# Kernel optimization log

Measured on AMD Instinct MI355X. Metric: run time of the kernel, lower is better.

Reference implementation:

```python
import jax, jax.numpy as jnp
import numpy as np

N = 524288   # frontier nodes processed this step
D = 8        # max_output_degree (padded children per node)
H = 64       # h_size
X = 128      # x_size


def setup_inputs() -> dict:
    key = jax.random.key(0)
    ks = jax.random.split(key, 8)
    x_embs = jax.random.normal(ks[0], (N, X), dtype=jnp.float32)
    # node-level input mask (1.0 where node has an input word, else 0.0)
    x_mask = (jax.random.uniform(ks[1], (N,)) > 0.3).astype(jnp.float32)
    # hidden states of the already-computed (child) nodes
    h_prev = jax.random.normal(ks[2], (N, H), dtype=jnp.float32)
    # padded child index lists + validity mask (variable out-degree)
    child_idx = jax.random.randint(ks[3], (N, D), 0, N, dtype=jnp.int64)
    child_mask = (jax.random.uniform(ks[4], (N, D)) > 0.5).astype(jnp.float32)
    # parameters
    W_in = jax.random.normal(ks[5], (X, H), dtype=jnp.float32) * 0.05
    b_in = jnp.zeros((H,), dtype=jnp.float32)
    U = jax.random.normal(ks[6], (D, H, H), dtype=jnp.float32) * 0.05  # positional child matrices
    b_aggr = jnp.zeros((H,), dtype=jnp.float32)
    return {
        "x_embs": x_embs, "x_mask": x_mask, "h_prev": h_prev,
        "child_mask": child_mask, "W_in": W_in, "b_in": b_in,
        "U": U, "b_aggr": b_aggr, "child_idx": child_idx,
    }


def reference(x_embs, x_mask, h_prev, child_mask, W_in, b_in, U, b_aggr, child_idx):
    # message + mailbox: gather child hidden states -> [N, D, H], mask padding
    neighbour_h = h_prev[child_idx] * child_mask[..., None]
    # reduce: positional (non-stationary) linear aggregation  h_aggr = sum_p U_p h_p + b
    h_aggr = jnp.einsum("npd,pde->ne", neighbour_h, U) + b_aggr
    # apply: input linear, masked, add aggregate, tanh
    h = (x_embs @ W_in + b_in) * x_mask[:, None] + h_aggr
    return jnp.tanh(h)
```

## Files before the change

### kernel.cpp

```cpp
#include <hip/hip_runtime.h>
#include <hip/hip_bf16.h>

typedef __bf16 bf16x8 __attribute__((ext_vector_type(8)));
typedef float  f32x4  __attribute__((ext_vector_type(4)));
typedef int    i32x4  __attribute__((ext_vector_type(4)));

#define K_N 524288
#define K_D 8
#define K_H 64
#define K_X 128

#define WS_PACKED_SHORTS 40960
#define WS_ZERO_OFF_B    81920
#define WS_HB_OFF_B      131072
#define WS_NEEDED_MED    82432
#define WS_NEEDED_BIG    (131072 + (size_t)K_N * K_H * 2)

__global__ __launch_bounds__(512) void treernn_prep(
    const float* __restrict__ h_prev,
    const float* __restrict__ W_in,
    const float* __restrict__ U,
    short* __restrict__ wsPacked,
    float* __restrict__ zerop,
    __bf16* __restrict__ hb)
{
    const int b = blockIdx.x;
    if (b < 81) {
        if (threadIdx.x >= 64) return;
        const int f = b;
        const int lane = threadIdx.x;
        if (f == 80) {
            zerop[lane] = 0.0f;
            zerop[lane + 64] = 0.0f;
            return;
        }
        const int g = lane >> 4;
        const int c = lane & 15;
        bf16x8 v;
        if (f < 16) {
            const int ks = f >> 2, ct = f & 3;
            #pragma unroll
            for (int j = 0; j < 8; ++j) {
                const int k = ks * 32 + 8 * g + j;
                v[j] = (__bf16)W_in[k * K_H + ct * 16 + c];
            }
        } else {
            const int f2 = f - 16;
            const int p = f2 >> 3, ks = (f2 >> 2) & 1, ct = f2 & 3;
            #pragma unroll
            for (int j = 0; j < 8; ++j) {
                const int k = ks * 32 + 8 * g + j;
                v[j] = (__bf16)U[p * K_H * K_H + k * K_H + ct * 16 + c];
            }
        }
        *reinterpret_cast<bf16x8*>(wsPacked + ((size_t)f * 64 + lane) * 8) = v;
    } else {
        const size_t tid = (size_t)(b - 81) * 512 + threadIdx.x;
        const f32x4* s = reinterpret_cast<const f32x4*>(h_prev) + 2 * tid;
        const f32x4 v0 = __builtin_nontemporal_load(s);
        const f32x4 v1 = __builtin_nontemporal_load(s + 1);
        bf16x8 o;
        #pragma unroll
        for (int j = 0; j < 4; ++j) {
            o[j]     = (__bf16)v0[j];
            o[j + 4] = (__bf16)v1[j];
        }
        reinterpret_cast<bf16x8*>(hb)[tid] = o;
    }
}

__global__ __launch_bounds__(512, 4) void treernn_main_bf16(
    const float* __restrict__ x_embs,
    const float* __restrict__ x_mask,
    const __bf16* __restrict__ hb,
    const float* __restrict__ child_mask,
    const float* __restrict__ b_in,
    const float* __restrict__ b_aggr,
    const int*   __restrict__ child_idx,
    const short* __restrict__ wsPacked,
    const float* __restrict__ zerop,
    float* __restrict__ out)
{
    __shared__ __align__(16) short lds[WS_PACKED_SHORTS];

    {
        const i32x4* src = reinterpret_cast<const i32x4*>(wsPacked);
        i32x4* dst = reinterpret_cast<i32x4*>(lds);
        #pragma unroll
        for (int i = 0; i < 10; ++i)
            dst[threadIdx.x + i * 512] = src[threadIdx.x + i * 512];
    }

    const int lane = threadIdx.x & 63;
    const int wave = threadIdx.x >> 6;
    const int g = lane >> 4;
    const int c = lane & 15;
    const int base = (blockIdx.x * 8 + wave) * 32;
    const bf16x8* zb = reinterpret_cast<const bf16x8*>(zerop);

    int   idxs[2][8];
    float cms[2][8];
    #pragma unroll
    for (int rt = 0; rt < 2; ++rt) {
        const int node = base + rt * 16 + c;
        const i32x4* ip = reinterpret_cast<const i32x4*>(child_idx + (size_t)node * K_D);
        const i32x4 i0 = __builtin_nontemporal_load(ip);
        const i32x4 i1 = __builtin_nontemporal_load(ip + 1);
        idxs[rt][0] = i0[0]; idxs[rt][1] = i0[1]; idxs[rt][2] = i0[2]; idxs[rt][3] = i0[3];
        idxs[rt][4] = i1[0]; idxs[rt][5] = i1[1]; idxs[rt][6] = i1[2]; idxs[rt][7] = i1[3];
        const f32x4* mp = reinterpret_cast<const f32x4*>(child_mask + (size_t)node * K_D);
        const f32x4 m0 = __builtin_nontemporal_load(mp);
        const f32x4 m1 = __builtin_nontemporal_load(mp + 1);
        cms[rt][0] = m0[0]; cms[rt][1] = m0[1]; cms[rt][2] = m0[2]; cms[rt][3] = m0[3];
        cms[rt][4] = m1[0]; cms[rt][5] = m1[1]; cms[rt][6] = m1[2]; cms[rt][7] = m1[3];
    }

    f32x4 xmv[2];
    float xmrow[2];
    #pragma unroll
    for (int rt = 0; rt < 2; ++rt) {
        xmv[rt] = *reinterpret_cast<const f32x4*>(x_mask + base + rt * 16 + 4 * g);
        xmrow[rt] = x_mask[base + rt * 16 + c];
    }

    bf16x8 buf[3][2][2];

    #pragma unroll
    for (int rt = 0; rt < 2; ++rt) {
        const bf16x8* src = (cms[rt][0] != 0.0f)
            ? reinterpret_cast<const bf16x8*>(hb + (size_t)idxs[rt][0] * K_H) : zb;
        buf[0][rt][0] = src[g];
        buf[0][rt][1] = src[4 + g];
    }

    f32x4 acc[2][4];
    #pragma unroll
    for (int rt = 0; rt < 2; ++rt)
        #pragma unroll
        for (int ct = 0; ct < 4; ++ct) {
            f32x4 z = {0.0f, 0.0f, 0.0f, 0.0f};
            acc[rt][ct] = z;
        }

    __syncthreads();

    #pragma unroll
    for (int q = 1; q < 3; ++q) {
        #pragma unroll
        for (int rt = 0; rt < 2; ++rt) {
            const bf16x8* src = (cms[rt][q] != 0.0f)
                ? reinterpret_cast<const bf16x8*>(hb + (size_t)idxs[rt][q] * K_H) : zb;
            buf[q][rt][0] = src[g];
            buf[q][rt][1] = src[4 + g];
        }
    }

    {
        #pragma unroll
        for (int rt = 0; rt < 2; ++rt) {
            const float* src = (xmrow[rt] != 0.0f) ? (x_embs + (size_t)(base + rt * 16 + c) * K_X) : zerop;
            #pragma unroll
            for (int ks = 0; ks < 4; ++ks) {
                const f32x4 a0 = __builtin_nontemporal_load(reinterpret_cast<const f32x4*>(src + ks * 32 + 8 * g));
                const f32x4 a1 = __builtin_nontemporal_load(reinterpret_cast<const f32x4*>(src + ks * 32 + 8 * g + 4));
                bf16x8 af;
                #pragma unroll
                for (int j = 0; j < 4; ++j) {
                    af[j]     = (__bf16)a0[j];
                    af[j + 4] = (__bf16)a1[j];
                }
                #pragma unroll
                for (int ct = 0; ct < 4; ++ct) {
                    const bf16x8 wf = *reinterpret_cast<const bf16x8*>(&lds[((ks * 4 + ct) * 64 + lane) * 8]);
                    acc[rt][ct] = __builtin_amdgcn_mfma_f32_16x16x32_bf16(af, wf, acc[rt][ct], 0, 0, 0);
                }
            }
        }
    }

    #pragma unroll
    for (int p = 0; p < 8; ++p) {
        const int pb = p % 3;

        const bf16x8 a0_0 = buf[pb][0][0], a1_0 = buf[pb][0][1];
        const bf16x8 a0_1 = buf[pb][1][0], a1_1 = buf[pb][1][1];

        if (p < 5) {
            const int q = p + 3;
            #pragma unroll
            for (int rt = 0; rt < 2; ++rt) {
                const bf16x8* src = (cms[rt][q] != 0.0f)
                    ? reinterpret_cast<const bf16x8*>(hb + (size_t)idxs[rt][q] * K_H) : zb;
                buf[pb][rt][0] = src[g];
                buf[pb][rt][1] = src[4 + g];
            }
        }

        bf16x8 uf[2][4];
        #pragma unroll
        for (int ks = 0; ks < 2; ++ks)
            #pragma unroll
            for (int ct = 0; ct < 4; ++ct)
                uf[ks][ct] = *reinterpret_cast<const bf16x8*>(&lds[8192 + ((p * 8 + ks * 4 + ct) * 64 + lane) * 8]);

        #pragma unroll
        for (int ct = 0; ct < 4; ++ct)
            acc[0][ct] = __builtin_amdgcn_mfma_f32_16x16x32_bf16(a0_0, uf[0][ct], acc[0][ct], 0, 0, 0);
        #pragma unroll
        for (int ct = 0; ct < 4; ++ct)
            acc[0][ct] = __builtin_amdgcn_mfma_f32_16x16x32_bf16(a1_0, uf[1][ct], acc[0][ct], 0, 0, 0);
        #pragma unroll
        for (int ct = 0; ct < 4; ++ct)
            acc[1][ct] = __builtin_amdgcn_mfma_f32_16x16x32_bf16(a0_1, uf[0][ct], acc[1][ct], 0, 0, 0);
        #pragma unroll
        for (int ct = 0; ct < 4; ++ct)
            acc[1][ct] = __builtin_amdgcn_mfma_f32_16x16x32_bf16(a1_1, uf[1][ct], acc[1][ct], 0, 0, 0);
    }

    #pragma unroll
    for (int ct = 0; ct < 4; ++ct) {
        const int col = ct * 16 + c;
        const float bi = b_in[col];
        const float ba = b_aggr[col];
        #pragma unroll
        for (int rt = 0; rt < 2; ++rt) {
            #pragma unroll
            for (int j = 0; j < 4; ++j) {
                const int node = base + rt * 16 + 4 * g + j;
                const float xm = xmv[rt][j];
                float h = acc[rt][ct][j] + ba + ((xm != 0.0f) ? bi : 0.0f);
                h = fminf(fmaxf(h, -9.0f), 9.0f);
                const float ex = __expf(2.0f * h);
                __builtin_nontemporal_store((ex - 1.0f) / (ex + 1.0f), &out[(size_t)node * K_H + col]);
            }
        }
    }
}

__global__ void treernn_naive(
    const float* __restrict__ x_embs, const float* __restrict__ x_mask,
    const float* __restrict__ h_prev, const float* __restrict__ child_mask,
    const float* __restrict__ W_in,   const float* __restrict__ b_in,
    const float* __restrict__ U,      const float* __restrict__ b_aggr,
    const int*   __restrict__ child_idx, float* __restrict__ out)
{
    const int n = blockIdx.x * 4 + (threadIdx.x >> 6);
    const int e = threadIdx.x & 63;
    if (n >= K_N) return;
    float s = 0.0f;
    const float xm = x_mask[n];
    if (xm != 0.0f) {
        for (int k = 0; k < K_X; ++k) s += x_embs[(size_t)n * K_X + k] * W_in[k * K_H + e];
        s += b_in[e];
    }
    float a = b_aggr[e];
    for (int p = 0; p < K_D; ++p) {
        const float cm = child_mask[n * K_D + p];
        if (cm != 0.0f) {
            const int id = child_idx[n * K_D + p];
            const float* hp = h_prev + (size_t)id * K_H;
            for (int d = 0; d < K_H; ++d) a += hp[d] * U[p * K_H * K_H + d * K_H + e];
        }
    }
    float h = s + a;
    h = fminf(fmaxf(h, -9.0f), 9.0f);
    const float ex = __expf(2.0f * h);
    out[(size_t)n * K_H + e] = (ex - 1.0f) / (ex + 1.0f);
}

extern "C" void kernel_launch(void* const* d_in, const int* in_sizes, int n_in,
                              void* d_out, int out_size, void* d_ws, size_t ws_size,
                              hipStream_t stream) {
    const float* x_embs     = (const float*)d_in[0];
    const float* x_mask     = (const float*)d_in[1];
    const float* h_prev     = (const float*)d_in[2];
    const float* child_mask = (const float*)d_in[3];
    const float* W_in       = (const float*)d_in[4];
    const float* b_in       = (const float*)d_in[5];
    const float* U          = (const float*)d_in[6];
    const float* b_aggr     = (const float*)d_in[7];
    const int*   child_idx  = (const int*)d_in[8];
    float* out = (float*)d_out;

    if (d_ws != nullptr && ws_size >= WS_NEEDED_BIG) {
        short*  wsPacked = (short*)d_ws;
        float*  zerop    = (float*)((char*)d_ws + WS_ZERO_OFF_B);
        __bf16* hb       = (__bf16*)((char*)d_ws + WS_HB_OFF_B);
        treernn_prep<<<81 + K_N * K_H / 8 / 512, 512, 0, stream>>>(h_prev, W_in, U,
                                                                   wsPacked, zerop, hb);
        treernn_main_bf16<<<K_N / 256, 512, 0, stream>>>(x_embs, x_mask, hb, child_mask,
                                                         b_in, b_aggr, child_idx,
                                                         wsPacked, zerop, out);
    } else {
        treernn_naive<<<K_N / 4, 256, 0, stream>>>(x_embs, x_mask, h_prev, child_mask,
                                                   W_in, b_in, U, b_aggr, child_idx, out);
    }
}
```

Measured before the change: 163.9 us.

## Split prep kernel, drop nontemporal loads, shrink gather prefetch depth to two

Splits the combined prep kernel into a small weight-prepack kernel and a separate h_prev-to-bf16 conversion kernel. Replaces the nontemporal loads with plain loads for h_prev, child indices and masks. Cuts the child-state gather prefetch ring in the main kernel from three slots to two, which lowers register pressure but leaves less latency hiding for the random gathers. It also adds one more kernel launch.

```diff
diff --git a/kernel.cpp b/kernel.cpp
--- a/kernel.cpp
+++ b/kernel.cpp
@@ -16,57 +16,55 @@
 #define WS_NEEDED_MED    82432
 #define WS_NEEDED_BIG    (131072 + (size_t)K_N * K_H * 2)
 
-__global__ __launch_bounds__(512) void treernn_prep(
-    const float* __restrict__ h_prev,
+__global__ __launch_bounds__(64) void treernn_prepack(
     const float* __restrict__ W_in,
     const float* __restrict__ U,
     short* __restrict__ wsPacked,
-    float* __restrict__ zerop,
+    float* __restrict__ zerop)
+{
+    const int f = blockIdx.x;
+    const int lane = threadIdx.x;
+    if (f == 80) {
+        zerop[lane] = 0.0f;
+        zerop[lane + 64] = 0.0f;
+        return;
+    }
+    const int g = lane >> 4;
+    const int c = lane & 15;
+    bf16x8 v;
+    if (f < 16) {
+        const int ks = f >> 2, ct = f & 3;
+        #pragma unroll
+        for (int j = 0; j < 8; ++j) {
+            const int k = ks * 32 + 8 * g + j;
+            v[j] = (__bf16)W_in[k * K_H + ct * 16 + c];
+        }
+    } else {
+        const int f2 = f - 16;
+        const int p = f2 >> 3, ks = (f2 >> 2) & 1, ct = f2 & 3;
+        #pragma unroll
+        for (int j = 0; j < 8; ++j) {
+            const int k = ks * 32 + 8 * g + j;
+            v[j] = (__bf16)U[p * K_H * K_H + k * K_H + ct * 16 + c];
+        }
+    }
+    *reinterpret_cast<bf16x8*>(wsPacked + ((size_t)f * 64 + lane) * 8) = v;
+}
+
+__global__ __launch_bounds__(512) void treernn_h2bf16(
+    const float* __restrict__ h_prev,
     __bf16* __restrict__ hb)
 {
-    const int b = blockIdx.x;
-    if (b < 81) {
-        if (threadIdx.x >= 64) return;
-        const int f = b;
-        const int lane = threadIdx.x;
-        if (f == 80) {
-            zerop[lane] = 0.0f;
-            zerop[lane + 64] = 0.0f;
-            return;
-        }
-        const int g = lane >> 4;
-        const int c = lane & 15;
-        bf16x8 v;
-        if (f < 16) {
-            const int ks = f >> 2, ct = f & 3;
-            #pragma unroll
-            for (int j = 0; j < 8; ++j) {
-                const int k = ks * 32 + 8 * g + j;
-                v[j] = (__bf16)W_in[k * K_H + ct * 16 + c];
-            }
-        } else {
-            const int f2 = f - 16;
-            const int p = f2 >> 3, ks = (f2 >> 2) & 1, ct = f2 & 3;
-            #pragma unroll
-            for (int j = 0; j < 8; ++j) {
-                const int k = ks * 32 + 8 * g + j;
-                v[j] = (__bf16)U[p * K_H * K_H + k * K_H + ct * 16 + c];
-            }
-        }
-        *reinterpret_cast<bf16x8*>(wsPacked + ((size_t)f * 64 + lane) * 8) = v;
-    } else {
-        const size_t tid = (size_t)(b - 81) * 512 + threadIdx.x;
-        const f32x4* s = reinterpret_cast<const f32x4*>(h_prev) + 2 * tid;
-        const f32x4 v0 = __builtin_nontemporal_load(s);
-        const f32x4 v1 = __builtin_nontemporal_load(s + 1);
-        bf16x8 o;
-        #pragma unroll
-        for (int j = 0; j < 4; ++j) {
-            o[j]     = (__bf16)v0[j];
-            o[j + 4] = (__bf16)v1[j];
-        }
-        reinterpret_cast<bf16x8*>(hb)[tid] = o;
-    }
+    const size_t tid = (size_t)blockIdx.x * 512 + threadIdx.x;
+    const f32x4* s = reinterpret_cast<const f32x4*>(h_prev) + 2 * tid;
+    const f32x4 v0 = s[0], v1 = s[1];
+    bf16x8 o;
+    #pragma unroll
+    for (int j = 0; j < 4; ++j) {
+        o[j]     = (__bf16)v0[j];
+        o[j + 4] = (__bf16)v1[j];
+    }
+    reinterpret_cast<bf16x8*>(hb)[tid] = o;
 }
 
 __global__ __launch_bounds__(512, 4) void treernn_main_bf16(
@@ -104,13 +102,11 @@
     for (int rt = 0; rt < 2; ++rt) {
         const int node = base + rt * 16 + c;
         const i32x4* ip = reinterpret_cast<const i32x4*>(child_idx + (size_t)node * K_D);
-        const i32x4 i0 = __builtin_nontemporal_load(ip);
-        const i32x4 i1 = __builtin_nontemporal_load(ip + 1);
+        const i32x4 i0 = ip[0], i1 = ip[1];
         idxs[rt][0] = i0[0]; idxs[rt][1] = i0[1]; idxs[rt][2] = i0[2]; idxs[rt][3] = i0[3];
         idxs[rt][4] = i1[0]; idxs[rt][5] = i1[1]; idxs[rt][6] = i1[2]; idxs[rt][7] = i1[3];
         const f32x4* mp = reinterpret_cast<const f32x4*>(child_mask + (size_t)node * K_D);
-        const f32x4 m0 = __builtin_nontemporal_load(mp);
-        const f32x4 m1 = __builtin_nontemporal_load(mp + 1);
+        const f32x4 m0 = mp[0], m1 = mp[1];
         cms[rt][0] = m0[0]; cms[rt][1] = m0[1]; cms[rt][2] = m0[2]; cms[rt][3] = m0[3];
         cms[rt][4] = m1[0]; cms[rt][5] = m1[1]; cms[rt][6] = m1[2]; cms[rt][7] = m1[3];
     }
@@ -123,7 +119,7 @@
         xmrow[rt] = x_mask[base + rt * 16 + c];
     }
 
-    bf16x8 buf[3][2][2];
+    bf16x8 buf[2][2][2];
 
     #pragma unroll
     for (int rt = 0; rt < 2; ++rt) {
@@ -145,14 +141,11 @@
     __syncthreads();
 
     #pragma unroll
-    for (int q = 1; q < 3; ++q) {
-        #pragma unroll
-        for (int rt = 0; rt < 2; ++rt) {
-            const bf16x8* src = (cms[rt][q] != 0.0f)
-                ? reinterpret_cast<const bf16x8*>(hb + (size_t)idxs[rt][q] * K_H) : zb;
-            buf[q][rt][0] = src[g];
-            buf[q][rt][1] = src[4 + g];
-        }
+    for (int rt = 0; rt < 2; ++rt) {
+        const bf16x8* src = (cms[rt][1] != 0.0f)
+            ? reinterpret_cast<const bf16x8*>(hb + (size_t)idxs[rt][1] * K_H) : zb;
+        buf[1][rt][0] = src[g];
+        buf[1][rt][1] = src[4 + g];
     }
 
     {
@@ -180,13 +173,13 @@
 
     #pragma unroll
     for (int p = 0; p < 8; ++p) {
-        const int pb = p % 3;
+        const int pb = p & 1;
 
         const bf16x8 a0_0 = buf[pb][0][0], a1_0 = buf[pb][0][1];
         const bf16x8 a0_1 = buf[pb][1][0], a1_1 = buf[pb][1][1];
 
-        if (p < 5) {
-            const int q = p + 3;
+        if (p < 6) {
+            const int q = p + 2;
             #pragma unroll
             for (int rt = 0; rt < 2; ++rt) {
                 const bf16x8* src = (cms[rt][q] != 0.0f)
@@ -286,8 +279,8 @@
         short*  wsPacked = (short*)d_ws;
         float*  zerop    = (float*)((char*)d_ws + WS_ZERO_OFF_B);
         __bf16* hb       = (__bf16*)((char*)d_ws + WS_HB_OFF_B);
-        treernn_prep<<<81 + K_N * K_H / 8 / 512, 512, 0, stream>>>(h_prev, W_in, U,
-                                                                   wsPacked, zerop, hb);
+        treernn_prepack<<<81, 64, 0, stream>>>(W_in, U, wsPacked, zerop);
+        treernn_h2bf16<<<K_N * K_H / 8 / 512, 512, 0, stream>>>(h_prev, hb);
         treernn_main_bf16<<<K_N / 256, 512, 0, stream>>>(x_embs, x_mask, hb, child_mask,
                                                          b_in, b_aggr, child_idx,
                                                          wsPacked, zerop, out);
```

Result: faster. 154.9 us (-5.5%).
